# Kernel tuning notes

Hardware: AMD Instinct MI355X
Metric: run time of the kernel (lower is better)

## Reference

```python
import jax, jax.numpy as jnp
import numpy as np

DIM = 1024
HIDDEN = 2816
NUM_EXPERTS = 8
TOP_K = 2
BATCH, SEQ = 4, 2048


def setup_inputs() -> dict:
    key = jax.random.key(0)
    ks = jax.random.split(key, 5)
    x = jax.random.normal(ks[0], (BATCH, SEQ, DIM), dtype=jnp.float32)
    gate_w = jax.random.normal(ks[1], (NUM_EXPERTS, DIM), dtype=jnp.float32) * 0.02
    w1 = jax.random.normal(ks[2], (NUM_EXPERTS, HIDDEN, DIM), dtype=jnp.float32) * 0.02
    w3 = jax.random.normal(ks[3], (NUM_EXPERTS, HIDDEN, DIM), dtype=jnp.float32) * 0.02
    w2 = jax.random.normal(ks[4], (NUM_EXPERTS, DIM, HIDDEN), dtype=jnp.float32) * 0.02
    return {"x": x, "gate_w": gate_w, "w1": w1, "w3": w3, "w2": w2}


def reference(x, gate_w, w1, w3, w2):
    orig_shape = x.shape
    xf = x.reshape(-1, x.shape[-1])                      # [T, D]
    T = xf.shape[0]
    E, K = gate_w.shape[0], TOP_K

    # gating: softmax over experts, then top-k (descending, matches torch.topk)
    scores = jax.nn.softmax(xf @ gate_w.T, axis=-1)      # [T, E]
    expert_weights, expert_indices = jax.lax.top_k(scores, K)  # [T, K]
    expert_weights = expert_weights / jnp.sum(expert_weights, axis=-1, keepdims=True)

    # dispatch: each token duplicated K times (torch repeat_interleave)
    x_rep = jnp.repeat(xf, K, axis=0)                    # [T*K, D]
    flat_idx = expert_indices.reshape(-1)                # [T*K]

    # per-expert masked SwiGLU FFN, combined into y (loop over small fixed E)
    y = jnp.zeros_like(x_rep)
    for e in range(E):
        m = (flat_idx == e)[:, None]
        xe = jnp.where(m, x_rep, 0.0)                    # zero non-routed tokens
        h = jax.nn.silu(xe @ w1[e].T) * (xe @ w3[e].T)   # [T*K, H]
        out = h @ w2[e].T                                # [T*K, D]
        y = y + jnp.where(m, out, 0.0)

    # weighted combine over the K slots
    y = jnp.sum(y.reshape(T, K, -1) * expert_weights[..., None], axis=1)
    return y.reshape(orig_shape)
```

## Files before the change

### kernel.cpp

```cpp
#include <hip/hip_runtime.h>
#include <hip/hip_bf16.h>

#define NTOK 8192
#define DIM 1024
#define HID 2816
#define NE 8
#define NSLOT (NTOK*2)
#define BM 128
#define BK 32
#define MAXMT (NSLOT/BM + NE)

typedef float f32x4 __attribute__((ext_vector_type(4)));
typedef __bf16 bf16x8 __attribute__((ext_vector_type(8)));
typedef __bf16 bf16x4 __attribute__((ext_vector_type(4)));

#define MFMA(a,b,c) __builtin_amdgcn_mfma_f32_16x16x32_bf16(a,b,c,0,0,0)
#define SWZ(r,g) (((r)<<5) + ((((g) ^ (((r)>>1)&3)))<<3))

__device__ __forceinline__ void cvt_st8(__bf16* d, f32x4 a, f32x4 b){
  bf16x8 v;
  v[0]=(__bf16)a.x; v[1]=(__bf16)a.y; v[2]=(__bf16)a.z; v[3]=(__bf16)a.w;
  v[4]=(__bf16)b.x; v[5]=(__bf16)b.y; v[6]=(__bf16)b.z; v[7]=(__bf16)b.w;
  *reinterpret_cast<bf16x8*>(d) = v;
}
__device__ __forceinline__ void gld_lds16(const void* g, void* l){
  __builtin_amdgcn_global_load_lds(
    (const __attribute__((address_space(1))) void*)g,
    (__attribute__((address_space(3))) void*)l, 16, 0, 0);
}
__device__ __forceinline__ int xcd_map(int orig, int nwg){
  int q = nwg>>3, rr = nwg&7, x = orig&7, o = orig>>3;
  return (x<rr ? x*(q+1) : rr*(q+1)+(x-rr)*q) + o;
}

__global__ void k_zero(int* cnt){ if(threadIdx.x < NE) cnt[threadIdx.x] = 0; }

__global__ __launch_bounds__(256) void k_cvt3(
    const float* __restrict__ s1, const float* __restrict__ s3,
    const float* __restrict__ s2, __bf16* __restrict__ d1,
    __bf16* __restrict__ d3, __bf16* __restrict__ d2)
{
  const int PB = (NE*HID*DIM/8)/256;
  int seg = blockIdx.x / PB;
  int i   = (blockIdx.x % PB)*256 + threadIdx.x;
  const float* src = (seg==0) ? s1 : (seg==1) ? s3 : s2;
  __bf16*      dst = (seg==0) ? d1 : (seg==1) ? d3 : d2;
  const f32x4* s = reinterpret_cast<const f32x4*>(src) + (size_t)i*2;
  f32x4 a = s[0], b = s[1];
  cvt_st8(dst + (size_t)i*8, a, b);
}

__global__ __launch_bounds__(256) void k_gate(const float* __restrict__ x,
    const float* __restrict__ gw, int* __restrict__ idxs,
    float* __restrict__ wt, int* __restrict__ cnt, __bf16* __restrict__ xb)
{
  __shared__ double part[8][8][4];
  __shared__ double lg[8][8];

  int tid = threadIdx.x;
  int tl = tid>>5, e = (tid>>2)&7, q = tid&3;
  int t  = blockIdx.x*8 + tl;

  const f32x4* x4 = reinterpret_cast<const f32x4*>(x)  + (size_t)t*256 + q*64;
  const f32x4* g4 = reinterpret_cast<const f32x4*>(gw) + e*256 + q*64;

  double s0 = 0.0, s1 = 0.0;
#pragma unroll 4
  for(int j=0;j<64;j+=2){
    f32x4 a0 = x4[j],   b0 = g4[j];
    f32x4 a1 = x4[j+1], b1 = g4[j+1];
    s0 += (double)a0.x*b0.x + (double)a0.y*b0.y
        + (double)a0.z*b0.z + (double)a0.w*b0.w;
    s1 += (double)a1.x*b1.x + (double)a1.y*b1.y
        + (double)a1.z*b1.z + (double)a1.w*b1.w;
  }
  part[tl][e][q] = s0 + s1;
  __syncthreads();
  if(q==0)
    lg[tl][e] = part[tl][e][0] + part[tl][e][1] + part[tl][e][2] + part[tl][e][3];
  __syncthreads();

  if(tid < 8){
    int tt = blockIdx.x*8 + tid;
    int i1=0; double m1=lg[tid][0];
#pragma unroll
    for(int k=1;k<NE;k++) if(lg[tid][k]>m1){ m1=lg[tid][k]; i1=k; }
    int i2=-1; double m2=-1e300;
#pragma unroll
    for(int k=0;k<NE;k++) if(k!=i1 && lg[tid][k]>m2){ m2=lg[tid][k]; i2=k; }
    float e2 = __expf((float)(m2-m1));
    float w0 = 1.f/(1.f+e2);
    idxs[2*tt]=i1; idxs[2*tt+1]=i2;
    wt[2*tt]=w0;   wt[2*tt+1]=e2*w0;
    atomicAdd(&cnt[i1],1); atomicAdd(&cnt[i2],1);
  }

  const f32x4* xs = reinterpret_cast<const f32x4*>(x) + (size_t)blockIdx.x*2048;
  __bf16* xo = xb + (size_t)blockIdx.x*8192;
#pragma unroll
  for(int k=0;k<4;k++){
    int c = k*256 + tid;
    cvt_st8(xo + (size_t)c*8, xs[2*c], xs[2*c+1]);
  }
}

__global__ void k_prep(const int* __restrict__ cnt, int* __restrict__ off,
                       int* __restrict__ mtp, int* __restrict__ cursor)
{
  if(threadIdx.x==0){
    int o=0, m=0; off[0]=0; mtp[0]=0;
    for(int e=0;e<NE;e++){
      cursor[e]=o; o += cnt[e]; off[e+1]=o;
      m += (cnt[e]+BM-1)/BM;  mtp[e+1]=m;
    }
  }
}

__global__ __launch_bounds__(256) void k_scatter(const int* __restrict__ idxs,
    int* __restrict__ cursor, int* __restrict__ order, int* __restrict__ inv)
{
  int t = blockIdx.x*blockDim.x + threadIdx.x;
#pragma unroll
  for(int k=0;k<2;k++){
    int s = 2*t+k;
    int e = idxs[s];
    int p = atomicAdd(&cursor[e],1);
    order[p]=s; inv[s]=p;
  }
}

#define NT_H 11
__global__ __launch_bounds__(512) void k_ffn1(
    const __bf16* __restrict__ xb, const __bf16* __restrict__ w1b,
    const __bf16* __restrict__ w3b, const int* __restrict__ off,
    const int* __restrict__ mtp, const int* __restrict__ order,
    __bf16* __restrict__ h, int nt_off)
{
  __shared__ __align__(16) __bf16 lA [2][BM*BK];
  __shared__ __align__(16) __bf16 lB1[2][BM*BK];
  __shared__ __align__(16) __bf16 lB3[2][BM*BK];

  int wg = xcd_map(blockIdx.x, MAXMT*NT_H);
  int mt = wg / NT_H, nt = nt_off + wg % NT_H;
  if (mt >= mtp[NE]) return;
  int e = 0;
  while (mt >= mtp[e+1]) e++;
  int row0    = off[e] + (mt - mtp[e])*BM;
  int row_end = off[e+1];
  int n0      = nt*128;

  int tid = threadIdx.x, lane = tid&63;
  int srow = tid>>2;
  int scol = ((tid&3) ^ ((srow>>1)&3))<<3;
  int arow = min(row0 + srow, row_end-1);
  int tok  = order[arow] >> 1;
  const __bf16* gA  = xb  + (size_t)tok*DIM + scol;
  const __bf16* gB1 = w1b + (size_t)e*HID*DIM + (size_t)(n0+srow)*DIM + scol;
  const __bf16* gB3 = w3b + (size_t)e*HID*DIM + (size_t)(n0+srow)*DIM + scol;
  int ldso = (tid>>6)<<9;

  int wm = (tid>>6)>>2, wn = (tid>>6)&3;
  int fr = lane & 15, gq = lane>>4;

  f32x4 acc1[4][2], acc3[4][2];
#pragma unroll
  for(int m=0;m<4;m++)
#pragma unroll
    for(int n=0;n<2;n++){ acc1[m][n]=f32x4{0.f,0.f,0.f,0.f}; acc3[m][n]=f32x4{0.f,0.f,0.f,0.f}; }

  gld_lds16(gA,  &lA [0][ldso]);
  gld_lds16(gB1, &lB1[0][ldso]);
  gld_lds16(gB3, &lB3[0][ldso]);
  __syncthreads();

  const int NK = DIM/BK;
  int buf=0;
  for(int kt=0; kt<NK; kt++){
    if(kt+1<NK){
      gld_lds16(gA  + (kt+1)*BK, &lA [buf^1][ldso]);
      gld_lds16(gB1 + (kt+1)*BK, &lB1[buf^1][ldso]);
      gld_lds16(gB3 + (kt+1)*BK, &lB3[buf^1][ldso]);
    }
    bf16x8 av[4], bv[2], cv[2];
#pragma unroll
    for(int m=0;m<4;m++) av[m]=*reinterpret_cast<const bf16x8*>(&lA[buf][SWZ(wm*64+m*16+fr, gq)]);
#pragma unroll
    for(int n=0;n<2;n++){
      bv[n]=*reinterpret_cast<const bf16x8*>(&lB1[buf][SWZ(wn*32+n*16+fr, gq)]);
      cv[n]=*reinterpret_cast<const bf16x8*>(&lB3[buf][SWZ(wn*32+n*16+fr, gq)]);
    }
#pragma unroll
    for(int m=0;m<4;m++)
#pragma unroll
      for(int n=0;n<2;n++){
        acc1[m][n]=MFMA(av[m],bv[n],acc1[m][n]);
        acc3[m][n]=MFMA(av[m],cv[n],acc3[m][n]);
      }
    __syncthreads();
    buf^=1;
  }

#pragma unroll
  for(int m=0;m<4;m++){
    int rbase = row0 + wm*64 + m*16 + (gq<<2);
#pragma unroll
    for(int r=0;r<4;r++){
      if(rbase+r < row_end){
        __bf16* hp = h + (size_t)(rbase+r)*HID + n0 + wn*32 + fr;
#pragma unroll
        for(int n=0;n<2;n++){
          float u = acc1[m][n][r], v = acc3[m][n][r];
          hp[n*16] = (__bf16)( (u/(1.f+__expf(-u))) * v );
        }
      }
    }
  }
}

__global__ __launch_bounds__(512) void k_ffn2(
    const __bf16* __restrict__ h, const __bf16* __restrict__ w2b,
    const int* __restrict__ off, const int* __restrict__ mtp,
    __bf16* __restrict__ ys)
{
  __shared__ __align__(16) __bf16 lA[2][128*BK];
  __shared__ __align__(16) __bf16 lB[2][256*BK];

  const int NT = DIM/256;
  int wg = xcd_map(blockIdx.x, MAXMT*NT);
  int mt = wg / NT, nt = wg % NT;
  if (mt >= mtp[NE]) return;
  int e = 0;
  while (mt >= mtp[e+1]) e++;
  int row0    = off[e] + (mt - mtp[e])*BM;
  int row_end = off[e+1];
  int n0      = nt*256;

  int tid = threadIdx.x, lane = tid&63;
  int srow = tid>>2;
  int scol = ((tid&3) ^ ((srow>>1)&3))<<3;
  int hrow = min(row0 + srow, NSLOT-1);
  const __bf16* gA  = h   + (size_t)hrow*HID + scol;
  const __bf16* gB0 = w2b + (size_t)e*DIM*HID + (size_t)(n0+srow)*HID + scol;
  const __bf16* gB1 = w2b + (size_t)e*DIM*HID + (size_t)(n0+srow+128)*HID + scol;
  int ldso = (tid>>6)<<9;

  int wm = (tid>>6)>>2, wn = (tid>>6)&3;
  int fr = lane & 15, gq = lane>>4;

  f32x4 acc[4][4];
#pragma unroll
  for(int m=0;m<4;m++)
#pragma unroll
    for(int n=0;n<4;n++) acc[m][n]=f32x4{0.f,0.f,0.f,0.f};

  gld_lds16(gA,  &lA[0][ldso]);
  gld_lds16(gB0, &lB[0][ldso]);
  gld_lds16(gB1, &lB[0][4096+ldso]);
  __syncthreads();

  const int NK = HID/BK;
  int buf=0;
  for(int kt=0; kt<NK; kt++){
    if(kt+1<NK){
      gld_lds16(gA  + (kt+1)*BK, &lA[buf^1][ldso]);
      gld_lds16(gB0 + (kt+1)*BK, &lB[buf^1][ldso]);
      gld_lds16(gB1 + (kt+1)*BK, &lB[buf^1][4096+ldso]);
    }
    bf16x8 av[4], bv[4];
#pragma unroll
    for(int m=0;m<4;m++) av[m]=*reinterpret_cast<const bf16x8*>(&lA[buf][SWZ(wm*64+m*16+fr, gq)]);
#pragma unroll
    for(int n=0;n<4;n++) bv[n]=*reinterpret_cast<const bf16x8*>(&lB[buf][SWZ(wn*64+n*16+fr, gq)]);
#pragma unroll
    for(int m=0;m<4;m++)
#pragma unroll
      for(int n=0;n<4;n++)
        acc[m][n]=MFMA(av[m],bv[n],acc[m][n]);
    __syncthreads();
    buf^=1;
  }

#pragma unroll
  for(int m=0;m<4;m++){
    int rbase = row0 + wm*64 + m*16 + (gq<<2);
#pragma unroll
    for(int r=0;r<4;r++){
      if(rbase+r < row_end){
        __bf16* yp = ys + (size_t)(rbase+r)*DIM + n0 + wn*64 + fr;
#pragma unroll
        for(int n=0;n<4;n++) yp[n*16] = (__bf16)acc[m][n][r];
      }
    }
  }
}

__global__ __launch_bounds__(256) void k_combine(
    const __bf16* __restrict__ ys, const int* __restrict__ inv,
    const float* __restrict__ wt, float* __restrict__ y)
{
  int t  = blockIdx.x;
  int p0 = inv[2*t], p1 = inv[2*t+1];
  float w0 = wt[2*t], w1v = wt[2*t+1];
  int d = threadIdx.x*4;
  const __bf16* r0 = ys + (size_t)p0*DIM + d;
  const __bf16* r1 = ys + (size_t)p1*DIM + d;
  f32x4 o;
#pragma unroll
  for(int j=0;j<4;j++) o[j] = w0*(float)r0[j] + w1v*(float)r1[j];
  *reinterpret_cast<f32x4*>(y + (size_t)t*DIM + d) = o;
}

extern "C" void kernel_launch(void* const* d_in, const int* in_sizes, int n_in,
                              void* d_out, int out_size, void* d_ws, size_t ws_size,
                              hipStream_t stream)
{
  const float* x  = (const float*)d_in[0];
  const float* gw = (const float*)d_in[1];
  const float* w1 = (const float*)d_in[2];
  const float* w3 = (const float*)d_in[3];
  const float* w2 = (const float*)d_in[4];
  float* y = (float*)d_out;
  char* ws = (char*)d_ws;

  int*   cnt    = (int*)(ws + 0);
  int*   off    = (int*)(ws + 64);
  int*   mtp    = (int*)(ws + 128);
  int*   cursor = (int*)(ws + 256);
  int*   idxs   = (int*)(ws + 320);
  float* wt     = (float*)(ws + 320 + 65536);
  int*   order  = (int*)(ws + 320 + 2*65536);
  int*   inv    = (int*)(ws + 320 + 3*65536);
  __bf16* h     = (__bf16*)(ws + 262464);
  __bf16* xb    = (__bf16*)(ws + 262464 + 92274688ull);
  __bf16* w1b   = (__bf16*)(ws + 262464 + 92274688ull + 16777216ull);
  __bf16* w3b   = (__bf16*)(ws + 262464 + 92274688ull + 16777216ull + 46137344ull);
  __bf16* w2b   = (__bf16*)(ws + 262464 + 92274688ull + 16777216ull + 2*46137344ull);
  __bf16* ysb   = w1b;

  const int PB = (NE*HID*DIM/8)/256;

  k_zero   <<<1, 64, 0, stream>>>(cnt);
  k_gate   <<<NTOK/8, 256, 0, stream>>>(x, gw, idxs, wt, cnt, xb);
  k_prep   <<<1, 64, 0, stream>>>(cnt, off, mtp, cursor);
  k_scatter<<<NTOK/256, 256, 0, stream>>>(idxs, cursor, order, inv);
  k_cvt3   <<<3*PB, 256, 0, stream>>>(w1, w3, w2, w1b, w3b, w2b);
  k_ffn1   <<<MAXMT*NT_H, 512, 0, stream>>>(xb, w1b, w3b, off, mtp, order, h, 0);
  k_ffn1   <<<MAXMT*NT_H, 512, 0, stream>>>(xb, w1b, w3b, off, mtp, order, h, NT_H);
  k_ffn2   <<<MAXMT*(DIM/256), 512, 0, stream>>>(h, w2b, off, mtp, ysb);
  k_combine<<<NTOK, 256, 0, stream>>>(ysb, inv, wt, y);
}
```

Measured before the change: 659.4 us.

## Merge split ffn1 launches and shrink ffn2 tile to 128x128 with 256 threads

The two half-width k_ffn1 launches, each covering 11 column tiles, become one launch covering all 22 tiles of the hidden dimension. k_ffn2 goes from a 128x256 output tile with 8 waves to a 128x128 tile with 4 waves in a 2x2 layout; each thread now issues two A loads and two B loads per k-step. This aims to cut launch overhead and tail effects, and to give k_ffn2 twice as many workgroups for better CU occupancy. The cost is less reuse of A per workgroup and more redundant reads of h.

```diff
diff --git a/kernel.cpp b/kernel.cpp
--- a/kernel.cpp
+++ b/kernel.cpp
@@ -129,19 +129,19 @@
   }
 }
 
-#define NT_H 11
 __global__ __launch_bounds__(512) void k_ffn1(
     const __bf16* __restrict__ xb, const __bf16* __restrict__ w1b,
     const __bf16* __restrict__ w3b, const int* __restrict__ off,
     const int* __restrict__ mtp, const int* __restrict__ order,
-    __bf16* __restrict__ h, int nt_off)
+    __bf16* __restrict__ h)
 {
   __shared__ __align__(16) __bf16 lA [2][BM*BK];
   __shared__ __align__(16) __bf16 lB1[2][BM*BK];
   __shared__ __align__(16) __bf16 lB3[2][BM*BK];
 
-  int wg = xcd_map(blockIdx.x, MAXMT*NT_H);
-  int mt = wg / NT_H, nt = nt_off + wg % NT_H;
+  const int NT = HID/128;
+  int wg = xcd_map(blockIdx.x, MAXMT*NT);
+  int mt = wg / NT, nt = wg % NT;
   if (mt >= mtp[NE]) return;
   int e = 0;
   while (mt >= mtp[e+1]) e++;
@@ -217,15 +217,15 @@
   }
 }
 
-__global__ __launch_bounds__(512) void k_ffn2(
+__global__ __launch_bounds__(256) void k_ffn2(
     const __bf16* __restrict__ h, const __bf16* __restrict__ w2b,
     const int* __restrict__ off, const int* __restrict__ mtp,
     __bf16* __restrict__ ys)
 {
   __shared__ __align__(16) __bf16 lA[2][128*BK];
-  __shared__ __align__(16) __bf16 lB[2][256*BK];
-
-  const int NT = DIM/256;
+  __shared__ __align__(16) __bf16 lB[2][128*BK];
+
+  const int NT = DIM/128;
   int wg = xcd_map(blockIdx.x, MAXMT*NT);
   int mt = wg / NT, nt = wg % NT;
   if (mt >= mtp[NE]) return;
@@ -233,19 +233,21 @@
   while (mt >= mtp[e+1]) e++;
   int row0    = off[e] + (mt - mtp[e])*BM;
   int row_end = off[e+1];
-  int n0      = nt*256;
-
-  int tid = threadIdx.x, lane = tid&63;
+  int n0      = nt*128;
+
+  int tid = threadIdx.x, lane = tid&63, wave = tid>>6;
   int srow = tid>>2;
   int scol = ((tid&3) ^ ((srow>>1)&3))<<3;
-  int hrow = min(row0 + srow, NSLOT-1);
-  const __bf16* gA  = h   + (size_t)hrow*HID + scol;
+  int hr0 = min(row0 + srow,      NSLOT-1);
+  int hr1 = min(row0 + srow + 64, NSLOT-1);
+  const __bf16* gA0 = h   + (size_t)hr0*HID + scol;
+  const __bf16* gA1 = h   + (size_t)hr1*HID + scol;
   const __bf16* gB0 = w2b + (size_t)e*DIM*HID + (size_t)(n0+srow)*HID + scol;
-  const __bf16* gB1 = w2b + (size_t)e*DIM*HID + (size_t)(n0+srow+128)*HID + scol;
-  int ldso = (tid>>6)<<9;
-
-  int wm = (tid>>6)>>2, wn = (tid>>6)&3;
-  int fr = lane & 15, gq = lane>>4;
+  const __bf16* gB1 = w2b + (size_t)e*DIM*HID + (size_t)(n0+srow+64)*HID + scol;
+  int ldso = wave<<9;
+
+  int wm = wave>>1, wn = wave&1;
+  int fr = lane&15, gq = lane>>4;
 
   f32x4 acc[4][4];
 #pragma unroll
@@ -253,18 +255,20 @@
 #pragma unroll
     for(int n=0;n<4;n++) acc[m][n]=f32x4{0.f,0.f,0.f,0.f};
 
-  gld_lds16(gA,  &lA[0][ldso]);
+  gld_lds16(gA0, &lA[0][ldso]);
+  gld_lds16(gA1, &lA[0][2048+ldso]);
   gld_lds16(gB0, &lB[0][ldso]);
-  gld_lds16(gB1, &lB[0][4096+ldso]);
+  gld_lds16(gB1, &lB[0][2048+ldso]);
   __syncthreads();
 
   const int NK = HID/BK;
   int buf=0;
   for(int kt=0; kt<NK; kt++){
     if(kt+1<NK){
-      gld_lds16(gA  + (kt+1)*BK, &lA[buf^1][ldso]);
+      gld_lds16(gA0 + (kt+1)*BK, &lA[buf^1][ldso]);
+      gld_lds16(gA1 + (kt+1)*BK, &lA[buf^1][2048+ldso]);
       gld_lds16(gB0 + (kt+1)*BK, &lB[buf^1][ldso]);
-      gld_lds16(gB1 + (kt+1)*BK, &lB[buf^1][4096+ldso]);
+      gld_lds16(gB1 + (kt+1)*BK, &lB[buf^1][2048+ldso]);
     }
     bf16x8 av[4], bv[4];
 #pragma unroll
@@ -344,8 +348,7 @@
   k_prep   <<<1, 64, 0, stream>>>(cnt, off, mtp, cursor);
   k_scatter<<<NTOK/256, 256, 0, stream>>>(idxs, cursor, order, inv);
   k_cvt3   <<<3*PB, 256, 0, stream>>>(w1, w3, w2, w1b, w3b, w2b);
-  k_ffn1   <<<MAXMT*NT_H, 512, 0, stream>>>(xb, w1b, w3b, off, mtp, order, h, 0);
-  k_ffn1   <<<MAXMT*NT_H, 512, 0, stream>>>(xb, w1b, w3b, off, mtp, order, h, NT_H);
-  k_ffn2   <<<MAXMT*(DIM/256), 512, 0, stream>>>(h, w2b, off, mtp, ysb);
+  k_ffn1   <<<MAXMT*(HID/128), 512, 0, stream>>>(xb, w1b, w3b, off, mtp, order, h);
+  k_ffn2   <<<MAXMT*(DIM/128), 256, 0, stream>>>(h, w2b, off, mtp, ysb);
   k_combine<<<NTOK, 256, 0, stream>>>(ysb, inv, wt, y);
 }
```

Result: faster. 644.1 us (-2.3%).
